# Kernel optimization log

Hardware: AMD Instinct MI355X
Metric: run time of the kernel (lower is better)

## Reference

```python
import jax, jax.numpy as jnp
import numpy as np
from math import pi

RADIUS = 40.0  # radius_scale
B, N = 1, 512


def map_polar_sqr(x, y, eps=1e-9):
    r = jnp.sqrt(x * x + y * y + eps)
    cond1 = (x == 0.0) & (y == 0.0)
    cond2 = (jnp.abs(y) <= jnp.abs(x)) & (~cond1)
    sx = jnp.where(x == 0.0, 1.0, x)  # safe denominators
    sy = jnp.where(y == 0.0, 1.0, y)
    c = 4.0 / pi
    x2 = jnp.sign(x) * r
    y2 = c * jnp.sign(x) * r * jnp.arctan(y / sx)
    x3 = c * jnp.sign(y) * r * jnp.arctan(x / sy)
    y3 = jnp.sign(y) * r
    x_out = jnp.where(cond1, 0.0, jnp.where(cond2, x2, x3))
    y_out = jnp.where(cond1, 0.0, jnp.where(cond2, y2, y3))
    return x_out, y_out


def axis_weights(g, size):
    # F.grid_sample bilinear, align_corners=False, padding_mode='zeros':
    # pixel coord = ((g+1)*size - 1)/2; linear weights on floor/floor+1,
    # out-of-range taps drop to zero automatically (idx only covers 0..size-1).
    c = ((g + 1.0) * size - 1.0) * 0.5
    i0 = jnp.floor(c)
    f = c - i0
    idx = jnp.arange(size, dtype=g.dtype)
    m0 = (idx == i0[..., None]).astype(g.dtype)
    m1 = (idx == i0[..., None] + 1.0).astype(g.dtype)
    return (1.0 - f)[..., None] * m0 + f[..., None] * m1  # [..., size]


def cts_conv(kernel, field, center, feat, mask, radius):
    # kernel: [o, i, kD, kH, kW]; field/center: [b, n/m, 3]; feat: [b, n, i]; mask: [b, n, 1]
    rel = (field[:, None] - center[:, :, None]) / radius            # [b,m,n,3]
    r2 = jnp.sum(rel * rel, -1)                                     # [b,m,n]
    att = jax.nn.relu((1.0 - r2) ** 3)[..., None] * mask[:, None]   # [b,m,n,1]
    xs, ys = map_polar_sqr(rel[..., 0], rel[..., 1])
    zs = rel[..., 2]
    kD, kH, kW = kernel.shape[2:]
    # grid_sample coord order: grid x -> W (last dim), y -> H, z -> D (first spatial dim)
    wz = axis_weights(zs, kD)
    wy = axis_weights(ys, kH)
    wx = axis_weights(xs, kW)
    w = jnp.einsum('bmnz,bmny,bmnx->bmnzyx', wz, wy, wx)
    w = w.reshape(*w.shape[:3], -1)                                 # [b,m,n,g=kD*kH*kW]
    fa = feat[:, None] * att                                        # [b,m,n,i]
    # exact trilinear interp + neighbor contraction without the [b,m,n,o,i] tensor:
    t = jnp.einsum('bmng,bmni->bmgi', w, fa)                        # [b,m,g,i]
    K = kernel.reshape(kernel.shape[0], kernel.shape[1], -1)        # [o,i,g]
    return jnp.einsum('bmgi,oig->bmo', t, K)


def setup_inputs() -> dict:
    key = jax.random.key(0)
    ks = jax.random.split(key, 24)

    def kern(k, o, i):
        return (jax.random.uniform(k, (o, i, 4, 4, 4), dtype=jnp.float32) - 0.5) / float(np.sqrt(i))

    def lin(kw, kb, o, i):
        return (jax.random.normal(kw, (o, i), dtype=jnp.float32) * 0.05,
                jax.random.normal(kb, (o,), dtype=jnp.float32) * 0.05)

    p = jax.random.normal(ks[0], (B, N, 3), dtype=jnp.float32) * 20.0
    v = jax.random.normal(ks[1], (B, N, 3), dtype=jnp.float32)
    other_feats = jax.random.normal(ks[2], (B, N, 62), dtype=jnp.float32)
    fluid_mask = jnp.ones((B, N, 1), dtype=jnp.float32)

    k_fluid = kern(ks[3], 32, 66)
    Wf, bf = lin(ks[4], ks[5], 32, 66)
    k1 = kern(ks[6], 64, 64); W1, b1 = lin(ks[7], ks[8], 64, 64)
    k2 = kern(ks[9], 64, 64); W2, b2 = lin(ks[10], ks[11], 64, 64)
    k3 = kern(ks[12], 64, 64); W3, b3 = lin(ks[13], ks[14], 64, 64)
    k4 = kern(ks[15], 6, 64); W4, b4 = lin(ks[16], ks[17], 6, 64)
    return dict(p=p, v=v, other_feats=other_feats, fluid_mask=fluid_mask,
                k_fluid=k_fluid, Wf=Wf, bf=bf,
                k1=k1, W1=W1, b1=b1, k2=k2, W2=W2, b2=b2,
                k3=k3, W3=W3, b3=b3, k4=k4, W4=W4, b4=b4)


def reference(p, v, other_feats, fluid_mask, k_fluid, Wf, bf,
              k1, W1, b1, k2, W2, b2, k3, W3, b3, k4, W4, b4):
    feats0 = jnp.concatenate([jnp.ones_like(p[..., :1]), v, other_feats], -1)  # [b,n,66]
    oc = cts_conv(k_fluid, p, p, feats0, fluid_mask, RADIUS)
    od = feats0 @ Wf.T + bf
    output = jnp.concatenate([oc, od], -1)  # [b,n,64]
    for k, W, bb in ((k1, W1, b1), (k2, W2, b2), (k3, W3, b3), (k4, W4, b4)):
        h = jax.nn.relu(output)
        oc = cts_conv(k, p, p, h, fluid_mask, RADIUS)
        od = h @ W.T + bb
        if od.shape[-1] == output.shape[-1]:
            output = oc + od + output
        else:
            output = oc + od
    return output  # [b,n,6]
```

## Files before the change

### kernel.cpp

```cpp
#include <hip/hip_runtime.h>

typedef _Float16 f16;
typedef _Float16 f16x2 __attribute__((ext_vector_type(2)));
typedef _Float16 f16x8 __attribute__((ext_vector_type(8)));
typedef float f32x4 __attribute__((ext_vector_type(4)));

#define INV_R (1.0f / 40.0f)
#define NBLK 256

#define OFF_HTA  0u
#define OFF_HTB  81920u
#define OFF_KT0  163840u
#define OFF_KT1  720896u
#define OFF_KT2  1253376u
#define OFF_KT3  1785856u
#define OFF_KT4  2318336u
#define OFF_HG   2850816u
#define OFF_OG   2916352u
#define OFF_BAR  3047424u

#define PREP_TOTAL 1384448

__device__ __forceinline__ unsigned bar_ld(unsigned* p) {
  return __hip_atomic_load(p, __ATOMIC_RELAXED, __HIP_MEMORY_SCOPE_AGENT);
}
__device__ void gridbar(unsigned* bar, int phase) {
  __syncthreads();
  if (threadIdx.x == 0) {
    int bid = blockIdx.x;
    int xcd = bid & 7;
    unsigned* xcnt = bar + xcd * 32 + phase;
    unsigned* xrel = bar + 256 + xcd * 32 + phase;
    unsigned* gcnt = bar + 512 + phase;
    unsigned* grel = bar + 544 + phase;
    __threadfence();
    __hip_atomic_fetch_add(xcnt, 1u, __ATOMIC_RELAXED, __HIP_MEMORY_SCOPE_AGENT);
    if (bid < 8) {
      while (bar_ld(xcnt) < (NBLK / 8)) __builtin_amdgcn_s_sleep(2);
      __hip_atomic_fetch_add(gcnt, 1u, __ATOMIC_RELAXED, __HIP_MEMORY_SCOPE_AGENT);
      if (bid == 0) {
        while (bar_ld(gcnt) < 8u) __builtin_amdgcn_s_sleep(2);
        __hip_atomic_store(grel, 1u, __ATOMIC_RELAXED, __HIP_MEMORY_SCOPE_AGENT);
      } else {
        while (bar_ld(grel) == 0u) __builtin_amdgcn_s_sleep(2);
      }
      __hip_atomic_store(xrel, 1u, __ATOMIC_RELAXED, __HIP_MEMORY_SCOPE_AGENT);
    } else {
      while (bar_ld(xrel) == 0u) __builtin_amdgcn_s_sleep(4);
    }
    __threadfence();
  }
  __syncthreads();
}

__device__ __forceinline__ float feats0_val(int ch, int n, const float* v, const float* other) {
  if (ch == 0) return 1.0f;
  if (ch < 4) return v[n * 3 + (ch - 1)];
  return other[n * 62 + (ch - 4)];
}
__device__ __forceinline__ float atan_poly(float t) {
  float t2 = t * t;
  float p = -0.0117212f;
  p = p * t2 + 0.05265332f;
  p = p * t2 - 0.11643287f;
  p = p * t2 + 0.19354346f;
  p = p * t2 - 0.33262347f;
  p = p * t2 + 0.99997726f;
  return t * p;
}
__device__ __forceinline__ void axis_w(float g, int& i0c, int& i1c, float& w0, float& w1) {
  float c = 2.0f * g + 1.5f;
  float fl = floorf(c);
  float f = c - fl;
  int i0 = (int)fl;
  w0 = (i0 >= 0 && i0 <= 3) ? (1.0f - f) : 0.0f;
  w1 = (i0 >= -1 && i0 <= 2) ? f : 0.0f;
  i0c = min(max(i0, 0), 3);
  i1c = min(max(i0 + 1, 0), 3);
}
__device__ __forceinline__ float dot2f(f16x2 a, f16x2 b, float c) {
#if defined(__has_builtin) && __has_builtin(__builtin_amdgcn_fdot2)
  return __builtin_amdgcn_fdot2(a, b, c, false);
#else
  return c + (float)a[0] * (float)b[0] + (float)a[1] * (float)b[1];
#endif
}

__device__ void prep_body(const float* __restrict__ v, const float* __restrict__ other,
                          const float* __restrict__ kf, const float* __restrict__ Wf,
                          const float* __restrict__ k1, const float* __restrict__ W1,
                          const float* __restrict__ k2, const float* __restrict__ W2,
                          const float* __restrict__ k3, const float* __restrict__ W3,
                          const float* __restrict__ k4, const float* __restrict__ W4,
                          char* __restrict__ ws) {
  f16* hTA = (f16*)(ws + OFF_HTA);
  for (int idx = blockIdx.x * 256 + threadIdx.x; idx < PREP_TOTAL; idx += NBLK * 256) {
    int e = idx;
    if (e < 40960) {
      int i = e >> 9, n = e & 511;
      hTA[e] = (f16)((i < 66) ? feats0_val(i, n, v, other) : 0.0f);
      continue;
    }
    e -= 40960;
    if (e < 278528) {
      int o = (e >> 3) & 63;
      int k = ((e >> 9) << 3) + (e & 7);
      float val = 0.0f;
      if (k < 4224) { if (o < 32) val = kf[o * 4224 + k]; }
      else if (k < 4290) { if (o >= 32) val = Wf[(o - 32) * 66 + (k - 4224)]; }
      ((f16*)(ws + OFF_KT0))[e] = (f16)val;
      continue;
    }
    e -= 278528;
    if (e < 798720) {
      int which = e / 266240, ee = e % 266240;
      const float* kk = which == 0 ? k1 : (which == 1 ? k2 : k3);
      const float* WW = which == 0 ? W1 : (which == 1 ? W2 : W3);
      int o = (ee >> 3) & 63;
      int k = ((ee >> 9) << 3) + (ee & 7);
      float val = (k < 4096) ? kk[o * 4096 + k] : WW[o * 64 + (k - 4096)];
      ((f16*)(ws + OFF_KT1))[(size_t)which * 266240 + ee] = (f16)val;
      continue;
    }
    e -= 798720;
    {
      int o = (e >> 3) & 63;
      int k = ((e >> 9) << 3) + (e & 7);
      float val = 0.0f;
      if (o < 6) val = (k < 4096) ? k4[o * 4096 + k] : W4[o * 64 + (k - 4096)];
      ((f16*)(ws + OFF_KT4))[e] = (f16)val;
    }
  }
}

template<int LAYER>
__device__ void layer_body(const float* __restrict__ p, const float* __restrict__ mask,
                           const float* __restrict__ v, const float* __restrict__ other,
                           const float* __restrict__ bias, const f16* __restrict__ KT,
                           const f16* __restrict__ hT_in, f16* __restrict__ hT_out,
                           f16* __restrict__ hG, float* __restrict__ outG,
                           float* __restrict__ dout,
                           f16* __restrict__ Wl, f16* __restrict__ tt, float* __restrict__ red) {
  constexpr int CI     = (LAYER == 0) ? 66 : 64;
  constexpr int ITILES = (LAYER == 0) ? 5 : 4;
  constexpr int KD     = (LAYER == 0) ? 4352 : 4160;
  constexpr bool RES   = (LAYER >= 1 && LAYER <= 3);
  constexpr bool FINAL = (LAYER == 4);
  const int tid = threadIdx.x;
  const int b = blockIdx.x;
  const int wave = tid >> 6, lane = tid & 63;
  const int row = lane & 15, kgrp = lane >> 4;
  const int grow = wave * 16 + row;

  #pragma unroll
  for (int mi = 0; mi < 2; ++mi) {
    const int m = b + mi * NBLK;
    const float pmx = p[m * 3 + 0], pmy = p[m * 3 + 1], pmz = p[m * 3 + 2];
    f32x4 acc[ITILES];
    #pragma unroll
    for (int it = 0; it < ITILES; ++it) acc[it] = f32x4{0.f, 0.f, 0.f, 0.f};

    #pragma unroll
    for (int half = 0; half < 2; ++half) {
      __syncthreads();
      int4* w4 = (int4*)Wl;
      int4 z4 = make_int4(0, 0, 0, 0);
      #pragma unroll
      for (int i = 0; i < 8; ++i) w4[tid + i * 256] = z4;
      __syncthreads();
      {
        const int n = half * 256 + tid;
        float x = (p[n * 3 + 0] - pmx) * INV_R;
        float y = (p[n * 3 + 1] - pmy) * INV_R;
        float z = (p[n * 3 + 2] - pmz) * INV_R;
        float r2 = x * x + y * y + z * z;
        float q = 1.0f - r2;
        float att = (q > 0.0f) ? q * q * q * mask[n] : 0.0f;
        bool c1 = (x == 0.0f) && (y == 0.0f);
        bool c2 = (fabsf(y) <= fabsf(x)) && !c1;
        float r = sqrtf(x * x + y * y + 1e-9f);
        float num = c2 ? y : x;
        float den = c2 ? x : y;
        float a = atan_poly(num / den);
        float s2 = copysignf(r, x), s3 = copysignf(r, y);
        const float C4PI = 1.2732395447351628f;
        float xs = c1 ? 0.0f : (c2 ? s2 : C4PI * s3 * a);
        float ys = c1 ? 0.0f : (c2 ? C4PI * s2 * a : s3);
        float zs = z;
        int iz0, iz1, iy0, iy1, ix0, ix1;
        float wz0, wz1, wy0, wy1, wx0, wx1;
        axis_w(zs, iz0, iz1, wz0, wz1);
        axis_w(ys, iy0, iy1, wy0, wy1);
        axis_w(xs, ix0, ix1, wx0, wx1);
        wz0 *= att; wz1 *= att;
        int gz[2] = {iz0 * 16, iz1 * 16};
        int gy[2] = {iy0 * 4, iy1 * 4};
        int gx[2] = {ix0, ix1};
        float wzv[2] = {wz0, wz1}, wyv[2] = {wy0, wy1}, wxv[2] = {wx0, wx1};
        #pragma unroll
        for (int za = 0; za < 2; ++za)
          #pragma unroll
          for (int ya = 0; ya < 2; ++ya)
            #pragma unroll
            for (int xa = 0; xa < 2; ++xa) {
              float w = wzv[za] * wyv[ya] * wxv[xa];
              if (w != 0.0f) {
                int g = gz[za] + gy[ya] + gx[xa];
                Wl[g * 256 + (tid ^ ((g & 7) << 3))] = (f16)w;
              }
            }
      }
      __syncthreads();
      #pragma unroll
      for (int k0 = 0; k0 < 8; ++k0) {
        const int n0l = k0 * 32 + kgrp * 8;
        f16x8 afrag = *(f16x8*)&Wl[grow * 256 + (n0l ^ ((grow & 7) << 3))];
        #pragma unroll
        for (int it = 0; it < ITILES; ++it) {
          f16x8 bfrag = *(const f16x8*)&hT_in[(it * 16 + row) * 512 + half * 256 + n0l];
          acc[it] = __builtin_amdgcn_mfma_f32_16x16x32_f16(afrag, bfrag, acc[it], 0, 0, 0);
        }
      }
    }
    const int g4 = wave * 16 + kgrp * 4;
    #pragma unroll
    for (int it = 0; it < ITILES; ++it) {
      const int icol = it * 16 + row;
      if (icol < CI) {
        union { f16 h[4]; short4 s; } cv;
        #pragma unroll
        for (int r = 0; r < 4; ++r) cv.h[r] = (f16)acc[it][r];
        *(short4*)&tt[mi * 4352 + icol * 64 + g4] = cv.s;
      }
    }
    if (LAYER == 0) {
      if (tid < 128)
        tt[mi * 4352 + 4224 + tid] = (f16)((tid < 66) ? feats0_val(tid, m, v, other) : 0.0f);
    } else {
      if (tid < 64) tt[mi * 4352 + 4096 + tid] = hG[m * 64 + tid];
    }
  }
  __syncthreads();

  constexpr int GPS = KD / 32;
  {
    const int o = tid & 63, wv = tid >> 6;
    float a0 = 0.f, a1 = 0.f;
    const f16* kp  = KT + ((size_t)(wv * GPS) * 64 + o) * 8;
    const f16* t0p = tt + (size_t)(wv * GPS) * 8;
    const f16* t1p = tt + 4352 + (size_t)(wv * GPS) * 8;
    for (int g = 0; g < GPS; ++g) {
      union { f16x8 v8; f16x2 p2[4]; } uk, u0, u1;
      uk.v8 = *(const f16x8*)kp;
      u0.v8 = *(const f16x8*)t0p;
      u1.v8 = *(const f16x8*)t1p;
      kp += 512; t0p += 8; t1p += 8;
      #pragma unroll
      for (int j = 0; j < 4; ++j) {
        a0 = dot2f(uk.p2[j], u0.p2[j], a0);
        a1 = dot2f(uk.p2[j], u1.p2[j], a1);
      }
    }
    red[wv * 128 + o]      = a0;
    red[wv * 128 + 64 + o] = a1;
  }
  __syncthreads();
  if (tid < 128) {
    const int mi = tid >> 6, oo = tid & 63;
    const int m = b + mi * NBLK;
    float s = red[mi * 64 + oo] + red[128 + mi * 64 + oo]
            + red[256 + mi * 64 + oo] + red[384 + mi * 64 + oo];
    if (FINAL) {
      if (oo < 6) dout[m * 6 + oo] = s + bias[oo];
    } else {
      float bb = (LAYER == 0) ? ((oo < 32) ? 0.0f : bias[oo - 32]) : bias[oo];
      float val = s + bb;
      if (RES) val += outG[m * 64 + oo];
      outG[m * 64 + oo] = val;
      float h = fmaxf(val, 0.0f);
      hG[m * 64 + oo] = (f16)h;
      hT_out[oo * 512 + m] = (f16)h;
    }
  }
}

__global__ __launch_bounds__(256) void mega_kernel(
    const float* p, const float* v, const float* other, const float* mask,
    const float* kf, const float* Wf, const float* bf,
    const float* k1, const float* W1, const float* b1,
    const float* k2, const float* W2, const float* b2,
    const float* k3, const float* W3, const float* b3,
    const float* k4, const float* W4, const float* b4,
    float* dout, char* ws) {
  __shared__ int4 blob[3264];
  f16* Wl = (f16*)blob;
  f16* tt = Wl + 16384;
  float* red = (float*)(tt + 8704);
  unsigned* bar = (unsigned*)(ws + OFF_BAR);

  f16* hTA = (f16*)(ws + OFF_HTA);
  f16* hTB = (f16*)(ws + OFF_HTB);
  f16* hG  = (f16*)(ws + OFF_HG);
  float* outG = (float*)(ws + OFF_OG);

  prep_body(v, other, kf, Wf, k1, W1, k2, W2, k3, W3, k4, W4, ws);
  gridbar(bar, 0);
  layer_body<0>(p, mask, v, other, bf, (const f16*)(ws + OFF_KT0), hTA, hTB, hG, outG, nullptr, Wl, tt, red);
  gridbar(bar, 1);
  layer_body<1>(p, mask, v, other, b1, (const f16*)(ws + OFF_KT1), hTB, hTA, hG, outG, nullptr, Wl, tt, red);
  gridbar(bar, 2);
  layer_body<2>(p, mask, v, other, b2, (const f16*)(ws + OFF_KT2), hTA, hTB, hG, outG, nullptr, Wl, tt, red);
  gridbar(bar, 3);
  layer_body<3>(p, mask, v, other, b3, (const f16*)(ws + OFF_KT3), hTB, hTA, hG, outG, nullptr, Wl, tt, red);
  gridbar(bar, 4);
  layer_body<4>(p, mask, v, other, b4, (const f16*)(ws + OFF_KT4), hTA, nullptr, hG, outG, dout, Wl, tt, red);
}

__global__ __launch_bounds__(256) void prep_g(
    const float* v, const float* other, const float* kf, const float* Wf,
    const float* k1, const float* W1, const float* k2, const float* W2,
    const float* k3, const float* W3, const float* k4, const float* W4, char* ws) {
  prep_body(v, other, kf, Wf, k1, W1, k2, W2, k3, W3, k4, W4, ws);
}

template<int LAYER>
__global__ __launch_bounds__(256) void layer_g(
    const float* p, const float* mask, const float* v, const float* other,
    const float* bias, const f16* KT, const f16* hT_in, f16* hT_out,
    f16* hG, float* outG, float* dout) {
  __shared__ int4 blob[3264];
  f16* Wl = (f16*)blob;
  f16* tt = Wl + 16384;
  float* red = (float*)(tt + 8704);
  layer_body<LAYER>(p, mask, v, other, bias, KT, hT_in, hT_out, hG, outG, dout, Wl, tt, red);
}

extern "C" void kernel_launch(void* const* d_in, const int* in_sizes, int n_in,
                              void* d_out, int out_size, void* d_ws, size_t ws_size,
                              hipStream_t stream) {
  const float* p     = (const float*)d_in[0];
  const float* v     = (const float*)d_in[1];
  const float* other = (const float*)d_in[2];
  const float* mask  = (const float*)d_in[3];
  const float* kf    = (const float*)d_in[4];
  const float* Wf    = (const float*)d_in[5];
  const float* bf    = (const float*)d_in[6];
  const float* k1    = (const float*)d_in[7];
  const float* W1    = (const float*)d_in[8];
  const float* b1    = (const float*)d_in[9];
  const float* k2    = (const float*)d_in[10];
  const float* W2    = (const float*)d_in[11];
  const float* b2    = (const float*)d_in[12];
  const float* k3    = (const float*)d_in[13];
  const float* W3    = (const float*)d_in[14];
  const float* b3    = (const float*)d_in[15];
  const float* k4    = (const float*)d_in[16];
  const float* W4    = (const float*)d_in[17];
  const float* b4    = (const float*)d_in[18];
  float* dout = (float*)d_out;
  char* ws = (char*)d_ws;
  (void)in_sizes; (void)n_in; (void)out_size; (void)ws_size;

  const f16* KT0 = (const f16*)(ws + OFF_KT0);
  const f16* KT1 = (const f16*)(ws + OFF_KT1);
  const f16* KT2 = (const f16*)(ws + OFF_KT2);
  const f16* KT3 = (const f16*)(ws + OFF_KT3);
  const f16* KT4c = (const f16*)(ws + OFF_KT4);
  f16* hTA = (f16*)(ws + OFF_HTA);
  f16* hTB = (f16*)(ws + OFF_HTB);
  f16* hG  = (f16*)(ws + OFF_HG);
  float* outG = (float*)(ws + OFF_OG);

  int maxb = 0;
  hipError_t e1 = hipOccupancyMaxActiveBlocksPerMultiprocessor(
      &maxb, (const void*)mega_kernel, 256, 0);
  if (e1 == hipSuccess && maxb >= 1) {
    hipMemsetAsync(ws + OFF_BAR, 0, 2304, stream);
    void* args[] = {
      (void*)&p, (void*)&v, (void*)&other, (void*)&mask,
      (void*)&kf, (void*)&Wf, (void*)&bf,
      (void*)&k1, (void*)&W1, (void*)&b1,
      (void*)&k2, (void*)&W2, (void*)&b2,
      (void*)&k3, (void*)&W3, (void*)&b3,
      (void*)&k4, (void*)&W4, (void*)&b4,
      (void*)&dout, (void*)&ws
    };
    hipError_t e2 = hipLaunchCooperativeKernel((const void*)mega_kernel, dim3(NBLK),
                                               dim3(256), args, 0, stream);
    if (e2 == hipSuccess) return;
  }

  prep_g<<<NBLK, 256, 0, stream>>>(v, other, kf, Wf, k1, W1, k2, W2, k3, W3, k4, W4, ws);
  layer_g<0><<<NBLK, 256, 0, stream>>>(p, mask, v, other, bf, KT0, hTA, hTB, hG, outG, nullptr);
  layer_g<1><<<NBLK, 256, 0, stream>>>(p, mask, v, other, b1, KT1, hTB, hTA, hG, outG, nullptr);
  layer_g<2><<<NBLK, 256, 0, stream>>>(p, mask, v, other, b2, KT2, hTA, hTB, hG, outG, nullptr);
  layer_g<3><<<NBLK, 256, 0, stream>>>(p, mask, v, other, b3, KT3, hTB, hTA, hG, outG, nullptr);
  layer_g<4><<<NBLK, 256, 0, stream>>>(p, mask, v, other, b4, KT4c, hTA, nullptr, hG, outG, dout);
}
```

Baseline: 202.1 us.

## Use one block per query point with 512 blocks and lighter grid barrier

```diff
diff --git a/kernel.cpp b/kernel.cpp
--- a/kernel.cpp
+++ b/kernel.cpp
@@ -6,25 +6,36 @@
 typedef float f32x4 __attribute__((ext_vector_type(4)));
 
 #define INV_R (1.0f / 40.0f)
-#define NBLK 256
-
-#define OFF_HTA  0u
-#define OFF_HTB  81920u
-#define OFF_KT0  163840u
-#define OFF_KT1  720896u
-#define OFF_KT2  1253376u
-#define OFF_KT3  1785856u
-#define OFF_KT4  2318336u
-#define OFF_HG   2850816u
-#define OFF_OG   2916352u
-#define OFF_BAR  3047424u
+#define NBLK 512
+
+#define OFF_HT0  0u
+#define OFF_HT1  81920u
+#define OFF_HT2  163840u
+#define OFF_HT3  245760u
+#define OFF_HT4  327680u
+#define OFF_KT0  409600u
+#define OFF_KT1  966656u
+#define OFF_KT2  1499136u
+#define OFF_KT3  2031616u
+#define OFF_KT4  2564096u
+#define OFF_HG   3096576u
+#define OFF_OG   3162112u
+#define OFF_BAR  3293184u
 
 #define PREP_TOTAL 1384448
+
+__device__ __forceinline__ void st_sys_u16(void* p, unsigned v) {
+  asm volatile("global_store_short %0, %1, off sc0 sc1" :: "v"(p), "v"(v) : "memory");
+}
+__device__ __forceinline__ unsigned f16bits(float x) {
+  union { f16 h; unsigned short s; } cv; cv.h = (f16)x; return (unsigned)cv.s;
+}
 
 __device__ __forceinline__ unsigned bar_ld(unsigned* p) {
   return __hip_atomic_load(p, __ATOMIC_RELAXED, __HIP_MEMORY_SCOPE_AGENT);
 }
 __device__ void gridbar(unsigned* bar, int phase) {
+  asm volatile("s_waitcnt vmcnt(0)" ::: "memory");
   __syncthreads();
   if (threadIdx.x == 0) {
     int bid = blockIdx.x;
@@ -33,7 +44,6 @@
     unsigned* xrel = bar + 256 + xcd * 32 + phase;
     unsigned* gcnt = bar + 512 + phase;
     unsigned* grel = bar + 544 + phase;
-    __threadfence();
     __hip_atomic_fetch_add(xcnt, 1u, __ATOMIC_RELAXED, __HIP_MEMORY_SCOPE_AGENT);
     if (bid < 8) {
       while (bar_ld(xcnt) < (NBLK / 8)) __builtin_amdgcn_s_sleep(2);
@@ -48,7 +58,7 @@
     } else {
       while (bar_ld(xrel) == 0u) __builtin_amdgcn_s_sleep(4);
     }
-    __threadfence();
+    asm volatile("" ::: "memory");
   }
   __syncthreads();
 }
@@ -93,12 +103,12 @@
                           const float* __restrict__ k3, const float* __restrict__ W3,
                           const float* __restrict__ k4, const float* __restrict__ W4,
                           char* __restrict__ ws) {
-  f16* hTA = (f16*)(ws + OFF_HTA);
   for (int idx = blockIdx.x * 256 + threadIdx.x; idx < PREP_TOTAL; idx += NBLK * 256) {
     int e = idx;
     if (e < 40960) {
       int i = e >> 9, n = e & 511;
-      hTA[e] = (f16)((i < 66) ? feats0_val(i, n, v, other) : 0.0f);
+      float val = (i < 66) ? feats0_val(i, n, v, other) : 0.0f;
+      st_sys_u16((f16*)(ws + OFF_HT0) + e, f16bits(val));
       continue;
     }
     e -= 40960;
@@ -108,7 +118,7 @@
       float val = 0.0f;
       if (k < 4224) { if (o < 32) val = kf[o * 4224 + k]; }
       else if (k < 4290) { if (o >= 32) val = Wf[(o - 32) * 66 + (k - 4224)]; }
-      ((f16*)(ws + OFF_KT0))[e] = (f16)val;
+      st_sys_u16((f16*)(ws + OFF_KT0) + e, f16bits(val));
       continue;
     }
     e -= 278528;
@@ -119,7 +129,7 @@
       int o = (ee >> 3) & 63;
       int k = ((ee >> 9) << 3) + (ee & 7);
       float val = (k < 4096) ? kk[o * 4096 + k] : WW[o * 64 + (k - 4096)];
-      ((f16*)(ws + OFF_KT1))[(size_t)which * 266240 + ee] = (f16)val;
+      st_sys_u16((f16*)(ws + OFF_KT1) + (size_t)which * 266240 + ee, f16bits(val));
       continue;
     }
     e -= 798720;
@@ -128,7 +138,7 @@
       int k = ((e >> 9) << 3) + (e & 7);
       float val = 0.0f;
       if (o < 6) val = (k < 4096) ? k4[o * 4096 + k] : W4[o * 64 + (k - 4096)];
-      ((f16*)(ws + OFF_KT4))[e] = (f16)val;
+      st_sys_u16((f16*)(ws + OFF_KT4) + e, f16bits(val));
     }
   }
 }
@@ -147,129 +157,117 @@
   constexpr bool RES   = (LAYER >= 1 && LAYER <= 3);
   constexpr bool FINAL = (LAYER == 4);
   const int tid = threadIdx.x;
-  const int b = blockIdx.x;
+  const int m = blockIdx.x;
   const int wave = tid >> 6, lane = tid & 63;
   const int row = lane & 15, kgrp = lane >> 4;
   const int grow = wave * 16 + row;
 
+  const float pmx = p[m * 3 + 0], pmy = p[m * 3 + 1], pmz = p[m * 3 + 2];
+  f32x4 acc[ITILES];
   #pragma unroll
-  for (int mi = 0; mi < 2; ++mi) {
-    const int m = b + mi * NBLK;
-    const float pmx = p[m * 3 + 0], pmy = p[m * 3 + 1], pmz = p[m * 3 + 2];
-    f32x4 acc[ITILES];
+  for (int it = 0; it < ITILES; ++it) acc[it] = f32x4{0.f, 0.f, 0.f, 0.f};
+
+  #pragma unroll
+  for (int half = 0; half < 2; ++half) {
+    __syncthreads();
+    int4* w4 = (int4*)Wl;
+    int4 z4 = make_int4(0, 0, 0, 0);
     #pragma unroll
-    for (int it = 0; it < ITILES; ++it) acc[it] = f32x4{0.f, 0.f, 0.f, 0.f};
-
+    for (int i = 0; i < 8; ++i) w4[tid + i * 256] = z4;
+    __syncthreads();
+    {
+      const int n = half * 256 + tid;
+      float x = (p[n * 3 + 0] - pmx) * INV_R;
+      float y = (p[n * 3 + 1] - pmy) * INV_R;
+      float z = (p[n * 3 + 2] - pmz) * INV_R;
+      float r2 = x * x + y * y + z * z;
+      float q = 1.0f - r2;
+      float att = (q > 0.0f) ? q * q * q * mask[n] : 0.0f;
+      bool c1 = (x == 0.0f) && (y == 0.0f);
+      bool c2 = (fabsf(y) <= fabsf(x)) && !c1;
+      float r = sqrtf(x * x + y * y + 1e-9f);
+      float num = c2 ? y : x;
+      float den = c2 ? x : y;
+      float a = atan_poly(num / den);
+      float s2 = copysignf(r, x), s3 = copysignf(r, y);
+      const float C4PI = 1.2732395447351628f;
+      float xs = c1 ? 0.0f : (c2 ? s2 : C4PI * s3 * a);
+      float ys = c1 ? 0.0f : (c2 ? C4PI * s2 * a : s3);
+      float zs = z;
+      int iz0, iz1, iy0, iy1, ix0, ix1;
+      float wz0, wz1, wy0, wy1, wx0, wx1;
+      axis_w(zs, iz0, iz1, wz0, wz1);
+      axis_w(ys, iy0, iy1, wy0, wy1);
+      axis_w(xs, ix0, ix1, wx0, wx1);
+      wz0 *= att; wz1 *= att;
+      int gz[2] = {iz0 * 16, iz1 * 16};
+      int gy[2] = {iy0 * 4, iy1 * 4};
+      int gx[2] = {ix0, ix1};
+      float wzv[2] = {wz0, wz1}, wyv[2] = {wy0, wy1}, wxv[2] = {wx0, wx1};
+      #pragma unroll
+      for (int za = 0; za < 2; ++za)
+        #pragma unroll
+        for (int ya = 0; ya < 2; ++ya)
+          #pragma unroll
+          for (int xa = 0; xa < 2; ++xa) {
+            float w = wzv[za] * wyv[ya] * wxv[xa];
+            if (w != 0.0f) {
+              int g = gz[za] + gy[ya] + gx[xa];
+              Wl[g * 256 + (tid ^ ((g & 7) << 3))] = (f16)w;
+            }
+          }
+    }
+    __syncthreads();
     #pragma unroll
-    for (int half = 0; half < 2; ++half) {
-      __syncthreads();
-      int4* w4 = (int4*)Wl;
-      int4 z4 = make_int4(0, 0, 0, 0);
+    for (int k0 = 0; k0 < 8; ++k0) {
+      const int n0l = k0 * 32 + kgrp * 8;
+      f16x8 afrag = *(f16x8*)&Wl[grow * 256 + (n0l ^ ((grow & 7) << 3))];
       #pragma unroll
-      for (int i = 0; i < 8; ++i) w4[tid + i * 256] = z4;
-      __syncthreads();
-      {
-        const int n = half * 256 + tid;
-        float x = (p[n * 3 + 0] - pmx) * INV_R;
-        float y = (p[n * 3 + 1] - pmy) * INV_R;
-        float z = (p[n * 3 + 2] - pmz) * INV_R;
-        float r2 = x * x + y * y + z * z;
-        float q = 1.0f - r2;
-        float att = (q > 0.0f) ? q * q * q * mask[n] : 0.0f;
-        bool c1 = (x == 0.0f) && (y == 0.0f);
-        bool c2 = (fabsf(y) <= fabsf(x)) && !c1;
-        float r = sqrtf(x * x + y * y + 1e-9f);
-        float num = c2 ? y : x;
-        float den = c2 ? x : y;
-        float a = atan_poly(num / den);
-        float s2 = copysignf(r, x), s3 = copysignf(r, y);
-        const float C4PI = 1.2732395447351628f;
-        float xs = c1 ? 0.0f : (c2 ? s2 : C4PI * s3 * a);
-        float ys = c1 ? 0.0f : (c2 ? C4PI * s2 * a : s3);
-        float zs = z;
-        int iz0, iz1, iy0, iy1, ix0, ix1;
-        float wz0, wz1, wy0, wy1, wx0, wx1;
-        axis_w(zs, iz0, iz1, wz0, wz1);
-        axis_w(ys, iy0, iy1, wy0, wy1);
-        axis_w(xs, ix0, ix1, wx0, wx1);
-        wz0 *= att; wz1 *= att;
-        int gz[2] = {iz0 * 16, iz1 * 16};
-        int gy[2] = {iy0 * 4, iy1 * 4};
-        int gx[2] = {ix0, ix1};
-        float wzv[2] = {wz0, wz1}, wyv[2] = {wy0, wy1}, wxv[2] = {wx0, wx1};
-        #pragma unroll
-        for (int za = 0; za < 2; ++za)
-          #pragma unroll
-          for (int ya = 0; ya < 2; ++ya)
-            #pragma unroll
-            for (int xa = 0; xa < 2; ++xa) {
-              float w = wzv[za] * wyv[ya] * wxv[xa];
-              if (w != 0.0f) {
-                int g = gz[za] + gy[ya] + gx[xa];
-                Wl[g * 256 + (tid ^ ((g & 7) << 3))] = (f16)w;
-              }
-            }
+      for (int it = 0; it < ITILES; ++it) {
+        f16x8 bfrag = *(const f16x8*)&hT_in[(it * 16 + row) * 512 + half * 256 + n0l];
+        acc[it] = __builtin_amdgcn_mfma_f32_16x16x32_f16(afrag, bfrag, acc[it], 0, 0, 0);
       }
-      __syncthreads();
+    }
+  }
+  const int g4 = wave * 16 + kgrp * 4;
+  #pragma unroll
+  for (int it = 0; it < ITILES; ++it) {
+    const int icol = it * 16 + row;
+    if (icol < CI) {
+      union { f16 h[4]; short4 s; } cv;
       #pragma unroll
-      for (int k0 = 0; k0 < 8; ++k0) {
-        const int n0l = k0 * 32 + kgrp * 8;
-        f16x8 afrag = *(f16x8*)&Wl[grow * 256 + (n0l ^ ((grow & 7) << 3))];
-        #pragma unroll
-        for (int it = 0; it < ITILES; ++it) {
-          f16x8 bfrag = *(const f16x8*)&hT_in[(it * 16 + row) * 512 + half * 256 + n0l];
-          acc[it] = __builtin_amdgcn_mfma_f32_16x16x32_f16(afrag, bfrag, acc[it], 0, 0, 0);
-        }
-      }
-    }
-    const int g4 = wave * 16 + kgrp * 4;
-    #pragma unroll
-    for (int it = 0; it < ITILES; ++it) {
-      const int icol = it * 16 + row;
-      if (icol < CI) {
-        union { f16 h[4]; short4 s; } cv;
-        #pragma unroll
-        for (int r = 0; r < 4; ++r) cv.h[r] = (f16)acc[it][r];
-        *(short4*)&tt[mi * 4352 + icol * 64 + g4] = cv.s;
-      }
-    }
-    if (LAYER == 0) {
-      if (tid < 128)
-        tt[mi * 4352 + 4224 + tid] = (f16)((tid < 66) ? feats0_val(tid, m, v, other) : 0.0f);
-    } else {
-      if (tid < 64) tt[mi * 4352 + 4096 + tid] = hG[m * 64 + tid];
-    }
+      for (int r = 0; r < 4; ++r) cv.h[r] = (f16)acc[it][r];
+      *(short4*)&tt[icol * 64 + g4] = cv.s;
+    }
+  }
+  if (LAYER == 0) {
+    if (tid < 128)
+      tt[4224 + tid] = (f16)((tid < 66) ? feats0_val(tid, m, v, other) : 0.0f);
+  } else {
+    if (tid < 64) tt[4096 + tid] = hG[m * 64 + tid];
   }
   __syncthreads();
 
   constexpr int GPS = KD / 32;
   {
     const int o = tid & 63, wv = tid >> 6;
-    float a0 = 0.f, a1 = 0.f;
-    const f16* kp  = KT + ((size_t)(wv * GPS) * 64 + o) * 8;
-    const f16* t0p = tt + (size_t)(wv * GPS) * 8;
-    const f16* t1p = tt + 4352 + (size_t)(wv * GPS) * 8;
+    float a0 = 0.f;
+    const f16* kp = KT + ((size_t)(wv * GPS) * 64 + o) * 8;
+    const f16* tp = tt + (size_t)(wv * GPS) * 8;
     for (int g = 0; g < GPS; ++g) {
-      union { f16x8 v8; f16x2 p2[4]; } uk, u0, u1;
+      union { f16x8 v8; f16x2 p2[4]; } uk, u0;
       uk.v8 = *(const f16x8*)kp;
-      u0.v8 = *(const f16x8*)t0p;
-      u1.v8 = *(const f16x8*)t1p;
-      kp += 512; t0p += 8; t1p += 8;
+      u0.v8 = *(const f16x8*)tp;
+      kp += 512; tp += 8;
       #pragma unroll
-      for (int j = 0; j < 4; ++j) {
-        a0 = dot2f(uk.p2[j], u0.p2[j], a0);
-        a1 = dot2f(uk.p2[j], u1.p2[j], a1);
-      }
-    }
-    red[wv * 128 + o]      = a0;
-    red[wv * 128 + 64 + o] = a1;
+      for (int j = 0; j < 4; ++j) a0 = dot2f(uk.p2[j], u0.p2[j], a0);
+    }
+    red[wv * 64 + o] = a0;
   }
   __syncthreads();
-  if (tid < 128) {
-    const int mi = tid >> 6, oo = tid & 63;
-    const int m = b + mi * NBLK;
-    float s = red[mi * 64 + oo] + red[128 + mi * 64 + oo]
-            + red[256 + mi * 64 + oo] + red[384 + mi * 64 + oo];
+  if (tid < 64) {
+    const int oo = tid;
+    float s = red[oo] + red[64 + oo] + red[128 + oo] + red[192 + oo];
     if (FINAL) {
       if (oo < 6) dout[m * 6 + oo] = s + bias[oo];
     } else {
@@ -279,7 +277,7 @@
       outG[m * 64 + oo] = val;
       float h = fmaxf(val, 0.0f);
       hG[m * 64 + oo] = (f16)h;
-      hT_out[oo * 512 + m] = (f16)h;
+      st_sys_u16(&hT_out[oo * 512 + m], f16bits(h));
     }
   }
 }
@@ -292,28 +290,31 @@
     const float* k3, const float* W3, const float* b3,
     const float* k4, const float* W4, const float* b4,
     float* dout, char* ws) {
-  __shared__ int4 blob[3264];
+  __shared__ int4 blob[2656];
   f16* Wl = (f16*)blob;
   f16* tt = Wl + 16384;
-  float* red = (float*)(tt + 8704);
+  float* red = (float*)(tt + 4352);
   unsigned* bar = (unsigned*)(ws + OFF_BAR);
 
-  f16* hTA = (f16*)(ws + OFF_HTA);
-  f16* hTB = (f16*)(ws + OFF_HTB);
+  f16* hT0 = (f16*)(ws + OFF_HT0);
+  f16* hT1 = (f16*)(ws + OFF_HT1);
+  f16* hT2 = (f16*)(ws + OFF_HT2);
+  f16* hT3 = (f16*)(ws + OFF_HT3);
+  f16* hT4 = (f16*)(ws + OFF_HT4);
   f16* hG  = (f16*)(ws + OFF_HG);
   float* outG = (float*)(ws + OFF_OG);
 
   prep_body(v, other, kf, Wf, k1, W1, k2, W2, k3, W3, k4, W4, ws);
   gridbar(bar, 0);
-  layer_body<0>(p, mask, v, other, bf, (const f16*)(ws + OFF_KT0), hTA, hTB, hG, outG, nullptr, Wl, tt, red);
+  layer_body<0>(p, mask, v, other, bf, (const f16*)(ws + OFF_KT0), hT0, hT1, hG, outG, nullptr, Wl, tt, red);
   gridbar(bar, 1);
-  layer_body<1>(p, mask, v, other, b1, (const f16*)(ws + OFF_KT1), hTB, hTA, hG, outG, nullptr, Wl, tt, red);
+  layer_body<1>(p, mask, v, other, b1, (const f16*)(ws + OFF_KT1), hT1, hT2, hG, outG, nullptr, Wl, tt, red);
   gridbar(bar, 2);
-  layer_body<2>(p, mask, v, other, b2, (const f16*)(ws + OFF_KT2), hTA, hTB, hG, outG, nullptr, Wl, tt, red);
+  layer_body<2>(p, mask, v, other, b2, (const f16*)(ws + OFF_KT2), hT2, hT3, hG, outG, nullptr, Wl, tt, red);
   gridbar(bar, 3);
-  layer_body<3>(p, mask, v, other, b3, (const f16*)(ws + OFF_KT3), hTB, hTA, hG, outG, nullptr, Wl, tt, red);
+  layer_body<3>(p, mask, v, other, b3, (const f16*)(ws + OFF_KT3), hT3, hT4, hG, outG, nullptr, Wl, tt, red);
   gridbar(bar, 4);
-  layer_body<4>(p, mask, v, other, b4, (const f16*)(ws + OFF_KT4), hTA, nullptr, hG, outG, dout, Wl, tt, red);
+  layer_body<4>(p, mask, v, other, b4, (const f16*)(ws + OFF_KT4), hT4, nullptr, hG, outG, dout, Wl, tt, red);
 }
 
 __global__ __launch_bounds__(256) void prep_g(
@@ -328,10 +329,10 @@
     const float* p, const float* mask, const float* v, const float* other,
     const float* bias, const f16* KT, const f16* hT_in, f16* hT_out,
     f16* hG, float* outG, float* dout) {
-  __shared__ int4 blob[3264];
+  __shared__ int4 blob[2656];
   f16* Wl = (f16*)blob;
   f16* tt = Wl + 16384;
-  float* red = (float*)(tt + 8704);
+  float* red = (float*)(tt + 4352);
   layer_body<LAYER>(p, mask, v, other, bias, KT, hT_in, hT_out, hG, outG, dout, Wl, tt, red);
 }
 
@@ -366,15 +367,18 @@
   const f16* KT2 = (const f16*)(ws + OFF_KT2);
   const f16* KT3 = (const f16*)(ws + OFF_KT3);
   const f16* KT4c = (const f16*)(ws + OFF_KT4);
-  f16* hTA = (f16*)(ws + OFF_HTA);
-  f16* hTB = (f16*)(ws + OFF_HTB);
+  f16* hT0 = (f16*)(ws + OFF_HT0);
+  f16* hT1 = (f16*)(ws + OFF_HT1);
+  f16* hT2 = (f16*)(ws + OFF_HT2);
+  f16* hT3 = (f16*)(ws + OFF_HT3);
+  f16* hT4 = (f16*)(ws + OFF_HT4);
   f16* hG  = (f16*)(ws + OFF_HG);
   float* outG = (float*)(ws + OFF_OG);
 
   int maxb = 0;
   hipError_t e1 = hipOccupancyMaxActiveBlocksPerMultiprocessor(
       &maxb, (const void*)mega_kernel, 256, 0);
-  if (e1 == hipSuccess && maxb >= 1) {
+  if (e1 == hipSuccess && maxb >= 2) {
     hipMemsetAsync(ws + OFF_BAR, 0, 2304, stream);
     void* args[] = {
       (void*)&p, (void*)&v, (void*)&other, (void*)&mask,
@@ -391,9 +395,9 @@
   }
 
   prep_g<<<NBLK, 256, 0, stream>>>(v, other, kf, Wf, k1, W1, k2, W2, k3, W3, k4, W4, ws);
-  layer_g<0><<<NBLK, 256, 0, stream>>>(p, mask, v, other, bf, KT0, hTA, hTB, hG, outG, nullptr);
-  layer_g<1><<<NBLK, 256, 0, stream>>>(p, mask, v, other, b1, KT1, hTB, hTA, hG, outG, nullptr);
-  layer_g<2><<<NBLK, 256, 0, stream>>>(p, mask, v, other, b2, KT2, hTA, hTB, hG, outG, nullptr);
-  layer_g<3><<<NBLK, 256, 0, stream>>>(p, mask, v, other, b3, KT3, hTB, hTA, hG, outG, nullptr);
-  layer_g<4><<<NBLK, 256, 0, stream>>>(p, mask, v, other, b4, KT4c, hTA, nullptr, hG, outG, dout);
-}
+  layer_g<0><<<NBLK, 256, 0, stream>>>(p, mask, v, other, bf, KT0, hT0, hT1, hG, outG, nullptr);
+  layer_g<1><<<NBLK, 256, 0, stream>>>(p, mask, v, other, b1, KT1, hT1, hT2, hG, outG, nullptr);
+  layer_g<2><<<NBLK, 256, 0, stream>>>(p, mask, v, other, b2, KT2, hT2, hT3, hG, outG, nullptr);
+  layer_g<3><<<NBLK, 256, 0, stream>>>(p, mask, v, other, b3, KT3, hT3, hT4, hG, outG, nullptr);
+  layer_g<4><<<NBLK, 256, 0, stream>>>(p, mask, v, other, b4, KT4c, hT4, nullptr, hG, outG, dout);
+}
```

Result: faster. 185.4 us (-8.3%).
